# Performance work log

Measured on AMD Instinct MI355X. Metric: run time of the kernel, lower is better.

The kernel has to match this reference:

```python
import jax, jax.numpy as jnp
import numpy as np

N_V, N_H, T, B = 1024, 512, 128, 256


def setup_inputs() -> dict:
    key = jax.random.key(0)
    k = jax.random.split(key, 3)
    v_data = (jax.random.uniform(k[0], (N_V, T, B)) < 0.5).astype(jnp.float32)  # binary visibles
    W = 0.01 * jax.random.normal(k[1], (N_H, N_V), jnp.float32)
    U = 0.01 * jax.random.normal(k[2], (N_H, N_H), jnp.float32)
    b_h = jnp.zeros((N_H,), jnp.float32)
    b_init = jnp.zeros((N_H,), jnp.float32)
    b_v = jnp.zeros((N_V,), jnp.float32)
    return {"v_data": v_data, "W": W, "U": U, "b_h": b_h, "b_init": b_init,
            "b_v": b_v, "CDk": 2}


def _sample_r_over_time(v, W, U, b_h, b_init):
    # v: (V,T,B) -> r: (H,T,B). Sequential mean-field recurrence over T
    # (RTRBM._sample_r_given_v_over_time: t=0 uses b_init and U=0, t>0 uses U,b_h).
    Wv = jnp.einsum('hv,vtb->thb', W, v)  # (T,H,B)
    r0 = jax.nn.sigmoid(Wv[0] + b_init[:, None])

    def step(r_lag, wv_t):
        r_t = jax.nn.sigmoid(wv_t + U @ r_lag + b_h[:, None])
        return r_t, r_t

    _, rs = jax.lax.scan(step, r0, Wv[1:])
    r = jnp.concatenate([r0[None], rs], axis=0)  # (T,H,B)
    return jnp.transpose(r, (1, 0, 2))  # (H,T,B)


def _parallel_r(v, r_lagged, W, U, b_h, b_init):
    # RTRBM._parallel_sample_r_h_given_v probabilities; v:(V,T,B), r_lagged:(H,T,B)
    r0 = jax.nn.sigmoid(jnp.einsum('hv,vb->hb', W, v[:, 0]) + b_init[:, None])
    rr = jax.nn.sigmoid(jnp.einsum('hv,vtb->htb', W, v[:, 1:])
                        + jnp.einsum('hr,rtb->htb', U, r_lagged[:, :-1])
                        + b_h[:, None, None])
    return jnp.concatenate([r0[:, None], rr], axis=1)  # (H,T,B)


def reference(v_data, W, U, b_h, b_init, b_v, CDk):
    key = jax.random.key(42)
    r_data = _sample_r_over_time(v_data, W, U, b_h, b_init)
    key, sk = jax.random.split(key)
    h_model = jax.random.bernoulli(sk, _parallel_r(v_data, r_data, W, U, b_h, b_init)).astype(v_data.dtype)
    for _ in range(CDk - 1):  # CD-k Gibbs chain (CDk is a concrete Python int)
        key, k1, k2 = jax.random.split(key, 3)
        v_prob = jax.nn.sigmoid(jnp.einsum('hv,htb->vtb', W, h_model) + b_v[:, None, None])
        v_model = jax.random.bernoulli(k1, v_prob).astype(v_data.dtype)
        h_model = jax.random.bernoulli(k2, _parallel_r(v_model, r_data, W, U, b_h, b_init)).astype(v_data.dtype)
    key, kf = jax.random.split(key)
    v_model = jax.random.bernoulli(
        kf, jax.nn.sigmoid(jnp.einsum('hv,htb->vtb', W, h_model) + b_v[:, None, None])
    ).astype(v_data.dtype)
    return (v_model, r_data)
```

## Files before the change

### kernel.cpp

```cpp
#include <hip/hip_runtime.h>
#include <hip/hip_bf16.h>
#include <stdint.h>

typedef unsigned long long u64;
typedef uint32_t u32;
typedef __attribute__((ext_vector_type(8))) short bf16x8;
typedef __attribute__((ext_vector_type(4))) float f32x4;

#define NV 1024
#define NH 512
#define TT 128
#define BB 256
#define TBsz (TT*BB)
#define HTBsz (NH*TBsz)
#define VTBsz (NV*TBsz)
#define NWV (NV/64)
#define NWH (NH/64)
#define QCAP 1048576u
#define DELTA 5e-4

__host__ __device__ inline void tf2x32(uint32_t k0, uint32_t k1,
                                       uint32_t x0, uint32_t x1,
                                       uint32_t& o0, uint32_t& o1) {
  const uint32_t ks2 = k0 ^ k1 ^ 0x1BD11BDAu;
#define ROTL(x,d) (((x)<<(d))|((x)>>(32-(d))))
#define RND(r) { x0 += x1; x1 = ROTL(x1,r); x1 ^= x0; }
  x0 += k0;  x1 += k1;
  RND(13) RND(15) RND(26) RND(6)
  x0 += k1;  x1 += ks2 + 1u;
  RND(17) RND(29) RND(16) RND(24)
  x0 += ks2; x1 += k0 + 2u;
  RND(13) RND(15) RND(26) RND(6)
  x0 += k0;  x1 += k1 + 3u;
  RND(17) RND(29) RND(16) RND(24)
  x0 += k1;  x1 += ks2 + 4u;
  RND(13) RND(15) RND(26) RND(6)
  x0 += ks2; x1 += k0 + 5u;
  o0 = x0; o1 = x1;
#undef RND
#undef ROTL
}

__device__ inline double tf_uniform64(uint32_t k0, uint32_t k1, uint32_t i) {
  uint32_t o0, o1;
  tf2x32(k0, k1, 0u, i, o0, o1);
  uint32_t bits = o0 ^ o1;
  uint32_t fb = (bits >> 9) | 0x3f800000u;
  float f = __uint_as_float(fb) - 1.0f;
  return (double)f;
}

__device__ inline double sigmoid64(double x) { return 1.0 / (1.0 + exp(-x)); }

__global__ __launch_bounds__(256) void kcvt(const float* __restrict__ s,
                                            double* __restrict__ d, int n) {
  int i = blockIdx.x * 256 + threadIdx.x;
  if (i < n) d[i] = (double)s[i];
}

__global__ __launch_bounds__(256) void kprepU(const float* __restrict__ U,
                                              float4* __restrict__ UB) {
  int i = blockIdx.x * 256 + threadIdx.x;
  int r4 = i / NH;
  int h  = i % NH;
  const float* __restrict__ p = U + (size_t)h*NH + r4*4;
  UB[i] = make_float4(p[0], p[1], p[2], p[3]);
}

__global__ __launch_bounds__(256) void kprepA(const float* __restrict__ W,
                                              ushort* __restrict__ A1,
                                              ushort* __restrict__ A2) {
  int idx = blockIdx.x * 256 + threadIdx.x;
  int i    = idx & 7;
  int lane = (idx >> 3) & 63;
  int ks   = (idx >> 9) & 15;
  int vt   = idx >> 13;
  int h = ks*32 + ((lane >> 4) << 3) + i;
  int v = vt*16 + (lane & 15);
  float w = W[(size_t)h*NV + v];
  __hip_bfloat16 b1 = __float2bfloat16(w);
  float r = w - __bfloat162float(b1);
  __hip_bfloat16 b2 = __float2bfloat16(r);
  A1[idx] = *reinterpret_cast<ushort*>(&b1);
  A2[idx] = *reinterpret_cast<ushort*>(&b2);
}

__global__ __launch_bounds__(256) void kprepAW(const float* __restrict__ W,
                                               ushort* __restrict__ AW1,
                                               ushort* __restrict__ AW2) {
  int idx = blockIdx.x * 256 + threadIdx.x;
  int i    = idx & 7;
  int lane = (idx >> 3) & 63;
  int kt   = (idx >> 9) & 31;
  int ht   = idx >> 14;
  int h = ht*16 + (lane & 15);
  int v = kt*32 + ((lane >> 4) << 3) + i;
  float w = W[(size_t)h*NV + v];
  __hip_bfloat16 b1 = __float2bfloat16(w);
  float r = w - __bfloat162float(b1);
  __hip_bfloat16 b2 = __float2bfloat16(r);
  AW1[idx] = *reinterpret_cast<ushort*>(&b1);
  AW2[idx] = *reinterpret_cast<ushort*>(&b2);
}

__global__ __launch_bounds__(256) void kprepAU(const float* __restrict__ U,
                                               ushort* __restrict__ AU1,
                                               ushort* __restrict__ AU2) {
  int idx = blockIdx.x * 256 + threadIdx.x;
  int i    = idx & 7;
  int lane = (idx >> 3) & 63;
  int kt   = (idx >> 9) & 15;
  int ht   = idx >> 13;
  int h = ht*16 + (lane & 15);
  int r = kt*32 + ((lane >> 4) << 3) + i;
  float u = U[(size_t)h*NH + r];
  __hip_bfloat16 b1 = __float2bfloat16(u);
  float rs = u - __bfloat162float(b1);
  __hip_bfloat16 b2 = __float2bfloat16(rs);
  AU1[idx] = *reinterpret_cast<ushort*>(&b1);
  AU2[idx] = *reinterpret_cast<ushort*>(&b2);
}

__global__ __launch_bounds__(256) void kpack_f32(const float* __restrict__ in,
                                                 u64* __restrict__ out) {
  int tb = blockIdx.x * 256 + threadIdx.x;
  for (int w = 0; w < NWV; ++w) {
    u64 m = 0;
    #pragma unroll 8
    for (int j = 0; j < 64; ++j)
      m |= (u64)(in[(size_t)(w*64 + j)*TBsz + tb] != 0.0f ? 1 : 0) << j;
    out[(size_t)tb*NWV + w] = m;
  }
}

__global__ __launch_bounds__(256) void kWv(const u64* __restrict__ vb,
                                           const double* __restrict__ W64,
                                           double* __restrict__ WvT) {
  const int HM = 8;
  int t  = blockIdx.x / (NH/HM);
  int h0 = (blockIdx.x % (NH/HM)) * HM;
  int tb = t*BB + threadIdx.x;
  u64 m[NWV];
  #pragma unroll
  for (int w = 0; w < NWV; ++w) m[w] = vb[(size_t)tb*NWV + w];
  double acc[HM];
  #pragma unroll
  for (int i = 0; i < HM; ++i) acc[i] = 0.0;
  const double2* __restrict__ W2 = (const double2*)W64;
  for (int w = 0; w < NWV; ++w) {
    u64 mw = m[w];
    #pragma unroll 8
    for (int j2 = 0; j2 < 32; ++j2) {
      double bd0 = (double)((unsigned)((mw >> (2*j2+0)) & 1ull));
      double bd1 = (double)((unsigned)((mw >> (2*j2+1)) & 1ull));
      int vi = w*32 + j2;
      #pragma unroll
      for (int i = 0; i < HM; ++i) {
        double2 wv = W2[(size_t)(h0+i)*(NV/2) + vi];
        acc[i] = fma(bd0, wv.x, acc[i]);
        acc[i] = fma(bd1, wv.y, acc[i]);
      }
    }
  }
  #pragma unroll
  for (int i = 0; i < HM; ++i)
    WvT[(size_t)tb*NH + h0 + i] = acc[i];
}

__global__ __launch_bounds__(512) void krecur(const double* __restrict__ WvT,
                                              const float4* __restrict__ UB,
                                              const float* __restrict__ bh,
                                              const float* __restrict__ binit,
                                              double* __restrict__ rT) {
  __shared__ double rA[2][NH];
  const int b = blockIdx.x;
  const int h = threadIdx.x;
  const double bhd = (double)bh[h];
  double p = sigmoid64(WvT[(size_t)b*NH + h] + (double)binit[h]);
  rA[0][h] = p;
  rT[(size_t)b*NH + h] = p;
  __syncthreads();
  int cur = 0;
  for (int t = 1; t < TT; ++t) {
    double acc = WvT[((size_t)t*BB + b)*NH + h];
    double a0=0, a1=0, a2=0, a3=0;
    const double2* __restrict__ rA2 = (const double2*)rA[cur];
    #pragma unroll 4
    for (int r = 0; r < NH; r += 4) {
      float4 u4 = UB[(size_t)(r >> 2)*NH + h];
      double2 q01 = rA2[(r>>1)+0];
      double2 q23 = rA2[(r>>1)+1];
      a0 = fma((double)u4.x, q01.x, a0);
      a1 = fma((double)u4.y, q01.y, a1);
      a2 = fma((double)u4.z, q23.x, a2);
      a3 = fma((double)u4.w, q23.y, a3);
    }
    p = sigmoid64((acc + ((a0+a1)+(a2+a3))) + bhd);
    rA[cur ^ 1][h] = p;
    rT[((size_t)t*BB + b)*NH + h] = p;
    __syncthreads();
    cur ^= 1;
  }
}

__global__ __launch_bounds__(256) void ktrans_s(const double* __restrict__ rT,
                                                float* __restrict__ out_r,
                                                uint8_t* __restrict__ hbytes,
                                                u32 k0, u32 k1) {
  __shared__ double lds[32][33];
  int t  = blockIdx.x;
  int h0 = blockIdx.y * 32;
  int b0 = blockIdx.z * 32;
  int tx = threadIdx.x & 31;
  int ty = threadIdx.x >> 5;
  #pragma unroll
  for (int i = 0; i < 4; ++i) {
    int row = ty*4 + i;
    lds[row][tx] = rT[((size_t)t*BB + b0 + row)*NH + h0 + tx];
  }
  __syncthreads();
  #pragma unroll
  for (int i = 0; i < 4; ++i) {
    int row = ty*4 + i;
    out_r[(size_t)(h0+row)*TBsz + (size_t)t*BB + b0 + tx] = (float)lds[tx][row];
  }
  if (threadIdx.x < 128) {
    int tbr = threadIdx.x >> 2;
    int bix = threadIdx.x & 3;
    int tb  = t*BB + b0 + tbr;
    unsigned byte = 0;
    #pragma unroll
    for (int j = 0; j < 8; ++j) {
      int hrel = bix*8 + j;
      double p = lds[tbr][hrel];
      double u = tf_uniform64(k0, k1, (u32)((h0 + hrel)*TBsz + tb));
      byte |= (u < p) ? (1u << j) : 0u;
    }
    hbytes[(size_t)tb*(NH/8) + (h0 >> 3) + bix] = (uint8_t)byte;
  }
}

__global__ __launch_bounds__(256) void kvisM(
    const ushort* __restrict__ A1, const ushort* __restrict__ A2,
    const float* __restrict__ bv, const u64* __restrict__ hbits,
    u64* __restrict__ vbits, float* __restrict__ vf,
    u32* __restrict__ queue, u32* __restrict__ cnt, u32 k0, u32 k1) {
  __shared__ ushort Blds[64*512];
  int nblk = blockIdx.x & 511;
  int vblk = blockIdx.x >> 9;
  int tb0 = nblk * 64, v0 = vblk * 64;
  int tid = threadIdx.x;
  {
    int c = tid >> 2, seg = tid & 3;
    const u64* hp = hbits + (size_t)(tb0 + c)*NWH + seg*2;
    #pragma unroll
    for (int half = 0; half < 2; ++half) {
      u64 mm = hp[half];
      int kbase = seg*128 + half*64;
      #pragma unroll
      for (int j2 = 0; j2 < 32; ++j2) {
        int k = kbase + 2*j2;
        u32 val = (u32)((mm >> (2*j2)) & 1ull) * 0x3F80u
                | (u32)((mm >> (2*j2+1)) & 1ull) * 0x3F800000u;
        int blk = (k >> 3) ^ (c & 7);
        *(u32*)&Blds[c*512 + (blk << 3) + (k & 7)] = val;
      }
    }
  }
  __syncthreads();
  int wv = tid >> 6, l = tid & 63;
  int wr = wv >> 1, wc = wv & 1;
  f32x4 acc[2][2];
  #pragma unroll
  for (int m = 0; m < 2; ++m)
    #pragma unroll
    for (int n = 0; n < 2; ++n) acc[m][n] = (f32x4){0.f,0.f,0.f,0.f};
  for (int ks = 0; ks < 16; ++ks) {
    bf16x8 bf[2];
    #pragma unroll
    for (int n = 0; n < 2; ++n) {
      int col = wc*32 + n*16 + (l & 15);
      int k = ks*32 + ((l >> 4) << 3);
      int blk = (k >> 3) ^ (col & 7);
      bf[n] = *(const bf16x8*)&Blds[col*512 + (blk << 3)];
    }
    #pragma unroll
    for (int m = 0; m < 2; ++m) {
      int vt = vblk*4 + wr*2 + m;
      size_t abase = (((size_t)vt*16 + ks)*64 + l)*8;
      bf16x8 a1 = *(const bf16x8*)&A1[abase];
      bf16x8 a2 = *(const bf16x8*)&A2[abase];
      #pragma unroll
      for (int n = 0; n < 2; ++n) {
        acc[m][n] = __builtin_amdgcn_mfma_f32_16x16x32_bf16(a1, bf[n], acc[m][n], 0,0,0);
        acc[m][n] = __builtin_amdgcn_mfma_f32_16x16x32_bf16(a2, bf[n], acc[m][n], 0,0,0);
      }
    }
  }
  u64 mask[2] = {0, 0};
  int coln[2];
  #pragma unroll
  for (int n = 0; n < 2; ++n) {
    int col = wc*32 + n*16 + (l & 15);
    coln[n] = col;
    int tb = tb0 + col;
    #pragma unroll
    for (int m = 0; m < 2; ++m) {
      #pragma unroll
      for (int r = 0; r < 4; ++r) {
        int vrel = wr*32 + m*16 + ((l >> 4) << 2) + r;
        int v = v0 + vrel;
        float p = 1.f / (1.f + __expf(-(acc[m][n][r] + bv[v])));
        size_t o = (size_t)v*TBsz + tb;
        double u = tf_uniform64(k0, k1, (u32)o);
        double diff = (double)p - u;
        unsigned smp = diff > 0.0 ? 1u : 0u;
        if (fabs(diff) < DELTA) {
          u32 s = atomicAdd(cnt, 1u);
          if (s < QCAP) queue[s] = (u32)o;
        }
        if (smp) mask[n] |= 1ull << vrel;
        if (vf) vf[o] = (float)smp;
      }
    }
  }
  if (vbits) {
    __syncthreads();
    u64* sbits = (u64*)Blds;
    if (tid < 64) sbits[tid] = 0;
    __syncthreads();
    atomicOr(&sbits[coln[0]], mask[0]);
    atomicOr(&sbits[coln[1]], mask[1]);
    __syncthreads();
    if (tid < 64)
      vbits[(size_t)(tb0 + tid)*NWV + (v0 >> 6)] = sbits[tid];
  }
}

__global__ __launch_bounds__(256) void khidM(
    const ushort* __restrict__ AW1, const ushort* __restrict__ AW2,
    const ushort* __restrict__ AU1, const ushort* __restrict__ AU2,
    const float* __restrict__ bh, const float* __restrict__ binit,
    const u64* __restrict__ vbits, const float* __restrict__ r32,
    u64* __restrict__ h2bits, u32* __restrict__ queue,
    u32* __restrict__ cnt, u32 k0, u32 k1) {
  __shared__ ushort Blds[64*512];
  int nblk = blockIdx.x & 511;
  int hblk = blockIdx.x >> 9;
  int tb0 = nblk * 64, h0 = hblk * 64;
  int t = tb0 >> 8;
  int tid = threadIdx.x;
  int wv = tid >> 6, l = tid & 63;
  int wr = wv >> 1, wc = wv & 1;
  f32x4 acc[2][2];
  #pragma unroll
  for (int m = 0; m < 2; ++m)
    #pragma unroll
    for (int n = 0; n < 2; ++n) acc[m][n] = (f32x4){0.f,0.f,0.f,0.f};

  for (int q = 0; q < 2; ++q) {
    {
      int c = tid >> 2, seg = tid & 3;
      const u64* vp = vbits + (size_t)(tb0 + c)*NWV + q*8 + seg*2;
      #pragma unroll
      for (int half = 0; half < 2; ++half) {
        u64 mm = vp[half];
        int kbase = seg*128 + half*64;
        #pragma unroll
        for (int j2 = 0; j2 < 32; ++j2) {
          int k = kbase + 2*j2;
          u32 val = (u32)((mm >> (2*j2)) & 1ull) * 0x3F80u
                  | (u32)((mm >> (2*j2+1)) & 1ull) * 0x3F800000u;
          int blk = (k >> 3) ^ (c & 7);
          *(u32*)&Blds[c*512 + (blk << 3) + (k & 7)] = val;
        }
      }
    }
    __syncthreads();
    for (int ks = 0; ks < 16; ++ks) {
      int kt = q*16 + ks;
      bf16x8 bf[2];
      #pragma unroll
      for (int n = 0; n < 2; ++n) {
        int col = wc*32 + n*16 + (l & 15);
        int k = ks*32 + ((l >> 4) << 3);
        int blk = (k >> 3) ^ (col & 7);
        bf[n] = *(const bf16x8*)&Blds[col*512 + (blk << 3)];
      }
      #pragma unroll
      for (int m = 0; m < 2; ++m) {
        int ht = hblk*4 + wr*2 + m;
        size_t abase = (((size_t)ht*32 + kt)*64 + l)*8;
        bf16x8 a1 = *(const bf16x8*)&AW1[abase];
        bf16x8 a2 = *(const bf16x8*)&AW2[abase];
        #pragma unroll
        for (int n = 0; n < 2; ++n) {
          acc[m][n] = __builtin_amdgcn_mfma_f32_16x16x32_bf16(a1, bf[n], acc[m][n], 0,0,0);
          acc[m][n] = __builtin_amdgcn_mfma_f32_16x16x32_bf16(a2, bf[n], acc[m][n], 0,0,0);
        }
      }
    }
    __syncthreads();
  }

  if (t > 0) {
    int tbl0 = tb0 - 256;
    for (int pl = 0; pl < 2; ++pl) {
      {
        int c = tid >> 2, rseg = tid & 3;
        const float* rp = r32 + tbl0 + c;
        for (int rr = 0; rr < 128; ++rr) {
          int r = rseg*128 + rr;
          float x = rp[(size_t)r*TBsz];
          __hip_bfloat16 b1 = __float2bfloat16(x);
          ushort ub;
          if (pl == 0) {
            ub = *reinterpret_cast<ushort*>(&b1);
          } else {
            float res = x - __bfloat162float(b1);
            __hip_bfloat16 b2 = __float2bfloat16(res);
            ub = *reinterpret_cast<ushort*>(&b2);
          }
          int blk = (r >> 3) ^ (c & 7);
          Blds[c*512 + (blk << 3) + (r & 7)] = ub;
        }
      }
      __syncthreads();
      for (int ks = 0; ks < 16; ++ks) {
        bf16x8 bf[2];
        #pragma unroll
        for (int n = 0; n < 2; ++n) {
          int col = wc*32 + n*16 + (l & 15);
          int k = ks*32 + ((l >> 4) << 3);
          int blk = (k >> 3) ^ (col & 7);
          bf[n] = *(const bf16x8*)&Blds[col*512 + (blk << 3)];
        }
        #pragma unroll
        for (int m = 0; m < 2; ++m) {
          int ht = hblk*4 + wr*2 + m;
          size_t abase = (((size_t)ht*16 + ks)*64 + l)*8;
          bf16x8 a1 = *(const bf16x8*)&AU1[abase];
          bf16x8 a2 = *(const bf16x8*)&AU2[abase];
          #pragma unroll
          for (int n = 0; n < 2; ++n) {
            acc[m][n] = __builtin_amdgcn_mfma_f32_16x16x32_bf16(a1, bf[n], acc[m][n], 0,0,0);
            acc[m][n] = __builtin_amdgcn_mfma_f32_16x16x32_bf16(a2, bf[n], acc[m][n], 0,0,0);
          }
        }
      }
      __syncthreads();
    }
  }

  const float* __restrict__ bias = (t > 0) ? bh : binit;
  u64 mask[2] = {0, 0};
  int coln[2];
  #pragma unroll
  for (int n = 0; n < 2; ++n) {
    int col = wc*32 + n*16 + (l & 15);
    coln[n] = col;
    int tb = tb0 + col;
    #pragma unroll
    for (int m = 0; m < 2; ++m) {
      #pragma unroll
      for (int r = 0; r < 4; ++r) {
        int hrel = wr*32 + m*16 + ((l >> 4) << 2) + r;
        int h = h0 + hrel;
        float p = 1.f / (1.f + __expf(-(acc[m][n][r] + bias[h])));
        size_t o = (size_t)h*TBsz + tb;
        double u = tf_uniform64(k0, k1, (u32)o);
        double diff = (double)p - u;
        unsigned smp = diff > 0.0 ? 1u : 0u;
        if (fabs(diff) < DELTA) {
          u32 s = atomicAdd(cnt, 1u);
          if (s < QCAP) queue[s] = (u32)o;
        }
        if (smp) mask[n] |= 1ull << hrel;
      }
    }
  }
  __syncthreads();
  u64* sbits = (u64*)Blds;
  if (tid < 64) sbits[tid] = 0;
  __syncthreads();
  atomicOr(&sbits[coln[0]], mask[0]);
  atomicOr(&sbits[coln[1]], mask[1]);
  __syncthreads();
  if (tid < 64)
    h2bits[(size_t)(tb0 + tid)*NWH + hblk] = sbits[tid];
}

__global__ __launch_bounds__(256) void kvis_fix(
    const float* __restrict__ W, const float* __restrict__ bv,
    const u64* __restrict__ hbits, u64* __restrict__ fixbits,
    float* __restrict__ vf, const u32* __restrict__ queue,
    const u32* __restrict__ cnt, u32 k0, u32 k1) {
  u32 n = *cnt; if (n > QCAP) n = QCAP;
  for (u32 q = blockIdx.x*256 + threadIdx.x; q < n; q += gridDim.x*256) {
    u32 o = queue[q];
    u32 v = o / TBsz, tb = o % TBsz;
    double a0=0, a1=0, a2=0, a3=0;
    for (int w = 0; w < NWH; ++w) {
      u64 mw = hbits[(size_t)tb*NWH + w];
      for (int j = 0; j < 64; j += 4) {
        if ((mw >> (j+0)) & 1ull) a0 += (double)W[(size_t)(w*64+j+0)*NV + v];
        if ((mw >> (j+1)) & 1ull) a1 += (double)W[(size_t)(w*64+j+1)*NV + v];
        if ((mw >> (j+2)) & 1ull) a2 += (double)W[(size_t)(w*64+j+2)*NV + v];
        if ((mw >> (j+3)) & 1ull) a3 += (double)W[(size_t)(w*64+j+3)*NV + v];
      }
    }
    double p = sigmoid64(((a0+a1)+(a2+a3)) + (double)bv[v]);
    double u = tf_uniform64(k0, k1, o);
    unsigned smp = (u < p) ? 1u : 0u;
    if (vf) vf[o] = (float)smp;
    if (fixbits) {
      size_t wi = (size_t)tb*NWV + (v >> 6);
      unsigned bit = v & 63u;
      unsigned cur = (unsigned)((fixbits[wi] >> bit) & 1ull);
      if (cur != smp) atomicXor(&fixbits[wi], 1ull << bit);
    }
  }
}

__global__ __launch_bounds__(256) void khid_fix(
    const u64* __restrict__ vbits, const float* __restrict__ W,
    const double* __restrict__ U64, const float* __restrict__ bh,
    const float* __restrict__ binit, const double* __restrict__ rT,
    u64* __restrict__ fixbits, const u32* __restrict__ queue,
    const u32* __restrict__ cnt, u32 k0, u32 k1) {
  u32 n = *cnt; if (n > QCAP) n = QCAP;
  for (u32 q = blockIdx.x*256 + threadIdx.x; q < n; q += gridDim.x*256) {
    u32 o = queue[q];
    u32 h = o / TBsz, tb = o % TBsz;
    u32 t = tb / BB, b = tb % BB;
    double a0=0, a1=0, a2=0, a3=0;
    for (int w = 0; w < NWV; ++w) {
      u64 mw = vbits[(size_t)tb*NWV + w];
      for (int j = 0; j < 64; j += 4) {
        if ((mw >> (j+0)) & 1ull) a0 += (double)W[(size_t)h*NV + w*64+j+0];
        if ((mw >> (j+1)) & 1ull) a1 += (double)W[(size_t)h*NV + w*64+j+1];
        if ((mw >> (j+2)) & 1ull) a2 += (double)W[(size_t)h*NV + w*64+j+2];
        if ((mw >> (j+3)) & 1ull) a3 += (double)W[(size_t)h*NV + w*64+j+3];
      }
    }
    double logit = (a0+a1) + (a2+a3);
    if (t > 0) {
      const double* __restrict__ rp = rT + ((size_t)(t-1)*BB + b)*NH;
      const double* __restrict__ Ur = U64 + (size_t)h*NH;
      double u0=0, u1=0, u2=0, u3=0;
      for (int r = 0; r < NH; r += 4) {
        u0 = fma(Ur[r+0], rp[r+0], u0);
        u1 = fma(Ur[r+1], rp[r+1], u1);
        u2 = fma(Ur[r+2], rp[r+2], u2);
        u3 = fma(Ur[r+3], rp[r+3], u3);
      }
      logit = (logit + ((u0+u1)+(u2+u3))) + (double)bh[h];
    } else {
      logit += (double)binit[h];
    }
    double p = sigmoid64(logit);
    double u = tf_uniform64(k0, k1, o);
    unsigned smp = (u < p) ? 1u : 0u;
    size_t wi = (size_t)tb*NWH + (h >> 6);
    unsigned bit = h & 63u;
    unsigned cur = (unsigned)((fixbits[wi] >> bit) & 1ull);
    if (cur != smp) atomicXor(&fixbits[wi], 1ull << bit);
  }
}

extern "C" void kernel_launch(void* const* d_in, const int* in_sizes, int n_in,
                              void* d_out, int out_size, void* d_ws, size_t ws_size,
                              hipStream_t stream) {
  const float* vd    = (const float*)d_in[0];
  const float* W     = (const float*)d_in[1];
  const float* U     = (const float*)d_in[2];
  const float* bh    = (const float*)d_in[3];
  const float* binit = (const float*)d_in[4];
  const float* bv    = (const float*)d_in[5];

  float* out_v = (float*)d_out;
  float* out_r = (float*)d_out + VTBsz;
  double* WvT = (double*)d_out;

  char* w = (char*)d_ws;
  double* rT    = (double*)w;  w += (size_t)HTBsz*8;
  u64* vdbits   = (u64*)w;     w += (size_t)TBsz*NWV*8;
  u64* v1bits   = (u64*)w;     w += (size_t)TBsz*NWV*8;
  u64* h1bits   = (u64*)w;     w += (size_t)TBsz*NWH*8;
  u64* h2bits   = (u64*)w;     w += (size_t)TBsz*NWH*8;
  double* W64   = (double*)w;  w += (size_t)NH*NV*8;
  double* U64   = (double*)w;  w += (size_t)NH*NH*8;
  float4* UB    = (float4*)w;  w += (size_t)NH*NH*4;
  ushort* A1    = (ushort*)w;  w += (size_t)NH*NV*2;
  ushort* A2    = (ushort*)w;  w += (size_t)NH*NV*2;
  ushort* AW1   = (ushort*)w;  w += (size_t)NH*NV*2;
  ushort* AW2   = (ushort*)w;  w += (size_t)NH*NV*2;
  ushort* AU1   = (ushort*)w;  w += (size_t)NH*NH*2;
  ushort* AU2   = (ushort*)w;  w += (size_t)NH*NH*2;
  u32* q0       = (u32*)w;     w += (size_t)QCAP*4;
  u32* q1       = (u32*)w;     w += (size_t)QCAP*4;
  u32* q2       = (u32*)w;     w += (size_t)QCAP*4;
  u32* cnt      = (u32*)w;     w += 256;
  (void)ws_size; (void)in_sizes; (void)n_in; (void)out_size;

  uint32_t ka0,ka1, sk0,sk1;
  tf2x32(0u,42u, 0u,0u, ka0,ka1);
  tf2x32(0u,42u, 0u,1u, sk0,sk1);
  uint32_t kb0,kb1, k10,k11, k20,k21;
  tf2x32(ka0,ka1, 0u,0u, kb0,kb1);
  tf2x32(ka0,ka1, 0u,1u, k10,k11);
  tf2x32(ka0,ka1, 0u,2u, k20,k21);
  uint32_t kc0,kc1, kf0,kf1;
  tf2x32(kb0,kb1, 0u,0u, kc0,kc1);
  tf2x32(kb0,kb1, 0u,1u, kf0,kf1);

  hipMemsetAsync(cnt, 0, 3*sizeof(u32), stream);

  kcvt<<<(NH*NV+255)/256, 256, 0, stream>>>(W, W64, NH*NV);
  kcvt<<<(NH*NH+255)/256, 256, 0, stream>>>(U, U64, NH*NH);
  kprepU<<<(NH*NH/4)/256, 256, 0, stream>>>(U, UB);
  kprepA<<<(NH*NV)/256, 256, 0, stream>>>(W, A1, A2);
  kprepAW<<<(NH*NV)/256, 256, 0, stream>>>(W, AW1, AW2);
  kprepAU<<<(NH*NH)/256, 256, 0, stream>>>(U, AU1, AU2);
  kpack_f32<<<TBsz/256, 256, 0, stream>>>(vd, vdbits);

  kWv<<<TT*(NH/8), 256, 0, stream>>>(vdbits, W64, WvT);

  krecur<<<BB, NH, 0, stream>>>(WvT, UB, bh, binit, rT);

  ktrans_s<<<dim3(TT, NH/32, BB/32), 256, 0, stream>>>(rT, out_r,
                                                       (uint8_t*)h1bits, sk0, sk1);

  kvisM<<<16*512, 256, 0, stream>>>(A1, A2, bv, h1bits, v1bits, nullptr,
                                    q0, cnt+0, k10, k11);
  kvis_fix<<<128, 256, 0, stream>>>(W, bv, h1bits, v1bits, nullptr,
                                    q0, cnt+0, k10, k11);

  khidM<<<8*512, 256, 0, stream>>>(AW1, AW2, AU1, AU2, bh, binit,
                                   v1bits, out_r, h2bits, q1, cnt+1, k20, k21);
  khid_fix<<<128, 256, 0, stream>>>(v1bits, W, U64, bh, binit, rT,
                                    h2bits, q1, cnt+1, k20, k21);

  kvisM<<<16*512, 256, 0, stream>>>(A1, A2, bv, h2bits, nullptr, out_v,
                                    q2, cnt+2, kf0, kf1);
  kvis_fix<<<128, 256, 0, stream>>>(W, bv, h2bits, nullptr, out_v,
                                    q2, cnt+2, kf0, kf1);
}
```

Measured before the change: 5.023 ms.

## Merge weight prep kernels, split recurrence reads between LDS and global, remap r tile loads

Six weight-preparation kernels are merged into two, one for W and one for U, which cuts launch count and re-reads of W and U. In the sequential recurrence, the second half of the previous r vector is now read from global memory (rT) rather than LDS, spreading load across both memory paths. The r32 staging loop in a later kernel now maps thread ids to columns differently so that consecutive lanes read consecutive addresses. Reading rT right after other threads wrote it relies on the block barrier making global writes visible, which is a correctness risk.

```diff
diff --git a/kernel.cpp b/kernel.cpp
--- a/kernel.cpp
+++ b/kernel.cpp
@@ -52,73 +52,64 @@
 
 __device__ inline double sigmoid64(double x) { return 1.0 / (1.0 + exp(-x)); }
 
-__global__ __launch_bounds__(256) void kcvt(const float* __restrict__ s,
-                                            double* __restrict__ d, int n) {
-  int i = blockIdx.x * 256 + threadIdx.x;
-  if (i < n) d[i] = (double)s[i];
-}
-
-__global__ __launch_bounds__(256) void kprepU(const float* __restrict__ U,
-                                              float4* __restrict__ UB) {
-  int i = blockIdx.x * 256 + threadIdx.x;
-  int r4 = i / NH;
-  int h  = i % NH;
-  const float* __restrict__ p = U + (size_t)h*NH + r4*4;
-  UB[i] = make_float4(p[0], p[1], p[2], p[3]);
-}
-
-__global__ __launch_bounds__(256) void kprepA(const float* __restrict__ W,
-                                              ushort* __restrict__ A1,
-                                              ushort* __restrict__ A2) {
-  int idx = blockIdx.x * 256 + threadIdx.x;
-  int i    = idx & 7;
-  int lane = (idx >> 3) & 63;
-  int ks   = (idx >> 9) & 15;
-  int vt   = idx >> 13;
-  int h = ks*32 + ((lane >> 4) << 3) + i;
-  int v = vt*16 + (lane & 15);
-  float w = W[(size_t)h*NV + v];
+__device__ inline void bfsplit(float w, ushort& b1o, ushort& b2o) {
   __hip_bfloat16 b1 = __float2bfloat16(w);
   float r = w - __bfloat162float(b1);
   __hip_bfloat16 b2 = __float2bfloat16(r);
-  A1[idx] = *reinterpret_cast<ushort*>(&b1);
-  A2[idx] = *reinterpret_cast<ushort*>(&b2);
-}
-
-__global__ __launch_bounds__(256) void kprepAW(const float* __restrict__ W,
-                                               ushort* __restrict__ AW1,
-                                               ushort* __restrict__ AW2) {
+  b1o = *reinterpret_cast<ushort*>(&b1);
+  b2o = *reinterpret_cast<ushort*>(&b2);
+}
+
+__global__ __launch_bounds__(256) void kprepWall(const float* __restrict__ W,
+                                                 double* __restrict__ W64,
+                                                 ushort* __restrict__ A1,
+                                                 ushort* __restrict__ A2,
+                                                 ushort* __restrict__ AW1,
+                                                 ushort* __restrict__ AW2) {
   int idx = blockIdx.x * 256 + threadIdx.x;
-  int i    = idx & 7;
-  int lane = (idx >> 3) & 63;
-  int kt   = (idx >> 9) & 31;
-  int ht   = idx >> 14;
-  int h = ht*16 + (lane & 15);
-  int v = kt*32 + ((lane >> 4) << 3) + i;
-  float w = W[(size_t)h*NV + v];
-  __hip_bfloat16 b1 = __float2bfloat16(w);
-  float r = w - __bfloat162float(b1);
-  __hip_bfloat16 b2 = __float2bfloat16(r);
-  AW1[idx] = *reinterpret_cast<ushort*>(&b1);
-  AW2[idx] = *reinterpret_cast<ushort*>(&b2);
-}
-
-__global__ __launch_bounds__(256) void kprepAU(const float* __restrict__ U,
-                                               ushort* __restrict__ AU1,
-                                               ushort* __restrict__ AU2) {
+  W64[idx] = (double)W[idx];
+  {
+    int i    = idx & 7;
+    int lane = (idx >> 3) & 63;
+    int ks   = (idx >> 9) & 15;
+    int vt   = idx >> 13;
+    int h = ks*32 + ((lane >> 4) << 3) + i;
+    int v = vt*16 + (lane & 15);
+    bfsplit(W[(size_t)h*NV + v], A1[idx], A2[idx]);
+  }
+  {
+    int i    = idx & 7;
+    int lane = (idx >> 3) & 63;
+    int kt   = (idx >> 9) & 31;
+    int ht   = idx >> 14;
+    int h = ht*16 + (lane & 15);
+    int v = kt*32 + ((lane >> 4) << 3) + i;
+    bfsplit(W[(size_t)h*NV + v], AW1[idx], AW2[idx]);
+  }
+}
+
+__global__ __launch_bounds__(256) void kprepUall(const float* __restrict__ U,
+                                                 double* __restrict__ U64,
+                                                 float4* __restrict__ UB,
+                                                 ushort* __restrict__ AU1,
+                                                 ushort* __restrict__ AU2) {
   int idx = blockIdx.x * 256 + threadIdx.x;
-  int i    = idx & 7;
-  int lane = (idx >> 3) & 63;
-  int kt   = (idx >> 9) & 15;
-  int ht   = idx >> 13;
-  int h = ht*16 + (lane & 15);
-  int r = kt*32 + ((lane >> 4) << 3) + i;
-  float u = U[(size_t)h*NH + r];
-  __hip_bfloat16 b1 = __float2bfloat16(u);
-  float rs = u - __bfloat162float(b1);
-  __hip_bfloat16 b2 = __float2bfloat16(rs);
-  AU1[idx] = *reinterpret_cast<ushort*>(&b1);
-  AU2[idx] = *reinterpret_cast<ushort*>(&b2);
+  U64[idx] = (double)U[idx];
+  {
+    int i    = idx & 7;
+    int lane = (idx >> 3) & 63;
+    int kt   = (idx >> 9) & 15;
+    int ht   = idx >> 13;
+    int h = ht*16 + (lane & 15);
+    int r = kt*32 + ((lane >> 4) << 3) + i;
+    bfsplit(U[(size_t)h*NH + r], AU1[idx], AU2[idx]);
+  }
+  if (idx < NH*NH/4) {
+    int r4 = idx / NH;
+    int h  = idx % NH;
+    const float* __restrict__ p = U + (size_t)h*NH + r4*4;
+    UB[idx] = make_float4(p[0], p[1], p[2], p[3]);
+  }
 }
 
 __global__ __launch_bounds__(256) void kpack_f32(const float* __restrict__ in,
@@ -184,12 +175,24 @@
   for (int t = 1; t < TT; ++t) {
     double acc = WvT[((size_t)t*BB + b)*NH + h];
     double a0=0, a1=0, a2=0, a3=0;
-    const double2* __restrict__ rA2 = (const double2*)rA[cur];
+    const double2* __restrict__ xl = (const double2*)rA[cur];
+    const double2* __restrict__ xg =
+        (const double2*)(rT + ((size_t)(t-1)*BB + b)*NH);
     #pragma unroll 4
-    for (int r = 0; r < NH; r += 4) {
+    for (int r = 0; r < 256; r += 4) {
       float4 u4 = UB[(size_t)(r >> 2)*NH + h];
-      double2 q01 = rA2[(r>>1)+0];
-      double2 q23 = rA2[(r>>1)+1];
+      double2 q01 = xl[(r>>1)+0];
+      double2 q23 = xl[(r>>1)+1];
+      a0 = fma((double)u4.x, q01.x, a0);
+      a1 = fma((double)u4.y, q01.y, a1);
+      a2 = fma((double)u4.z, q23.x, a2);
+      a3 = fma((double)u4.w, q23.y, a3);
+    }
+    #pragma unroll 4
+    for (int r = 256; r < 512; r += 4) {
+      float4 u4 = UB[(size_t)(r >> 2)*NH + h];
+      double2 q01 = xg[(r>>1)+0];
+      double2 q23 = xg[(r>>1)+1];
       a0 = fma((double)u4.x, q01.x, a0);
       a1 = fma((double)u4.y, q01.y, a1);
       a2 = fma((double)u4.z, q23.x, a2);
@@ -407,10 +410,11 @@
     int tbl0 = tb0 - 256;
     for (int pl = 0; pl < 2; ++pl) {
       {
-        int c = tid >> 2, rseg = tid & 3;
-        const float* rp = r32 + tbl0 + c;
+        int c  = tid & 63;
+        int q4 = tid >> 6;
+        const float* __restrict__ rp = r32 + tbl0 + c;
         for (int rr = 0; rr < 128; ++rr) {
-          int r = rseg*128 + rr;
+          int r = q4*128 + rr;
           float x = rp[(size_t)r*TBsz];
           __hip_bfloat16 b1 = __float2bfloat16(x);
           ushort ub;
@@ -616,12 +620,8 @@
 
   hipMemsetAsync(cnt, 0, 3*sizeof(u32), stream);
 
-  kcvt<<<(NH*NV+255)/256, 256, 0, stream>>>(W, W64, NH*NV);
-  kcvt<<<(NH*NH+255)/256, 256, 0, stream>>>(U, U64, NH*NH);
-  kprepU<<<(NH*NH/4)/256, 256, 0, stream>>>(U, UB);
-  kprepA<<<(NH*NV)/256, 256, 0, stream>>>(W, A1, A2);
-  kprepAW<<<(NH*NV)/256, 256, 0, stream>>>(W, AW1, AW2);
-  kprepAU<<<(NH*NH)/256, 256, 0, stream>>>(U, AU1, AU2);
+  kprepWall<<<(NH*NV)/256, 256, 0, stream>>>(W, W64, A1, A2, AW1, AW2);
+  kprepUall<<<(NH*NH)/256, 256, 0, stream>>>(U, U64, UB, AU1, AU2);
   kpack_f32<<<TBsz/256, 256, 0, stream>>>(vd, vdbits);
 
   kWv<<<TT*(NH/8), 256, 0, stream>>>(vdbits, W64, WvT);
```

Measured after the change: 5.745 ms. +14.4%, slower.
